# Kernel tuning notes

Measured on AMD Instinct MI355X. Metric: run time of the kernel, lower is better.

Reference implementation:

```python
import jax, jax.numpy as jnp
import numpy as np

N_HEAD = 16
N_EMBD = 1024
HEAD_DIM = N_EMBD // N_HEAD
ROPE_BASE = 10000.0


def _rms_norm(x):
    # F.rms_norm with eps=None uses dtype eps
    eps = jnp.finfo(x.dtype).eps
    ms = jnp.mean(jnp.square(x), axis=-1, keepdims=True)
    return x * jax.lax.rsqrt(ms + eps)


def _rope_tables(T, dtype):
    inv_freq = 1.0 / (ROPE_BASE ** (jnp.arange(0, HEAD_DIM, 2, dtype=jnp.float32) / HEAD_DIM))
    t = jnp.arange(T, dtype=jnp.float32)
    freqs = jnp.outer(t, inv_freq)  # [T, D/2]
    cos = jnp.cos(freqs).astype(dtype)[None, :, None, :]  # [1,T,1,D/2]
    sin = jnp.sin(freqs).astype(dtype)[None, :, None, :]
    return cos, sin


def _apply_rotary(x, cos, sin):
    d = x.shape[-1] // 2
    x1, x2 = x[..., :d], x[..., d:]
    y1 = x1 * cos + x2 * sin
    y2 = -x1 * sin + x2 * cos
    return jnp.concatenate([y1, y2], axis=-1).astype(x.dtype)


def setup_inputs() -> dict:
    key = jax.random.key(0)
    ks = jax.random.split(key, 7)
    B, T, C = 4, 2048, N_EMBD
    s = 0.02
    return {
        "x": jax.random.normal(ks[0], (B, T, C), dtype=jnp.float32),
        "v1": jax.random.normal(ks[1], (B, T, C), dtype=jnp.float32),
        "Wq": jax.random.normal(ks[2], (C, C), dtype=jnp.float32) * s,
        "Wk": jax.random.normal(ks[3], (C, C), dtype=jnp.float32) * s,
        "Wv": jax.random.normal(ks[4], (C, C), dtype=jnp.float32) * s,
        "Wproj": jax.random.normal(ks[5], (C, C), dtype=jnp.float32) * s,
        "lamb": jnp.float32(0.5),
    }


def reference(x, v1, Wq, Wk, Wv, Wproj, lamb):
    B, T, C = x.shape
    H, D = N_HEAD, HEAD_DIM
    q = (x @ Wq.T).reshape(B, T, H, D)
    k = (x @ Wk.T).reshape(B, T, H, D)
    v = (x @ Wv.T).reshape(B, T, H, D)
    # value-lambda residual mix
    v = (1.0 - lamb) * v + lamb * v1.reshape(B, T, H, D)
    # RMSNorm then RoPE on q, k
    cos, sin = _rope_tables(T, x.dtype)
    q = _apply_rotary(_rms_norm(q), cos, sin)
    k = _apply_rotary(_rms_norm(k), cos, sin)
    # causal SDPA
    scale = 1.0 / jnp.sqrt(jnp.float32(D)).astype(x.dtype)
    scores = jnp.einsum("bthd,bshd->bhts", q, k) * scale  # [B,H,T,T]
    causal = jnp.tril(jnp.ones((T, T), dtype=bool))
    scores = jnp.where(causal[None, None], scores, jnp.finfo(scores.dtype).min)
    attn = jax.nn.softmax(scores, axis=-1)
    y = jnp.einsum("bhts,bshd->bthd", attn, v).reshape(B, T, C)
    y = y @ Wproj.T
    return (y, v1)
```

## Files before the change

kernel.cpp:

```cpp
#include <hip/hip_runtime.h>
#include <hip/hip_bf16.h>

typedef __bf16 bf16x8 __attribute__((ext_vector_type(8)));
typedef __bf16 bf16x4 __attribute__((ext_vector_type(4)));
typedef float  f32x4  __attribute__((ext_vector_type(4)));
typedef unsigned u32x4 __attribute__((ext_vector_type(4)));

#define B_ 4
#define T_ 2048
#define H_ 16
#define D_ 64
#define C_ 1024
#define M_ 8192
#define NE_ ((size_t)M_ * C_)
#define KVSTR_ 2048

__global__ void probe_dtype(const unsigned short* __restrict__ x,
                            int* __restrict__ flag)
{
  __shared__ float red[256];
  float m = 0.0f;
  for (int i = threadIdx.x; i < 4096; i += 256) {
    unsigned int u = ((unsigned int)x[i]) << 16;
    float v = fabsf(__uint_as_float(u));
    if (!(v <= 1e30f)) v = 1e31f;
    m = fmaxf(m, v);
  }
  red[threadIdx.x] = m;
  __syncthreads();
  for (int s = 128; s > 0; s >>= 1) {
    if (threadIdx.x < s) red[threadIdx.x] = fmaxf(red[threadIdx.x], red[threadIdx.x + s]);
    __syncthreads();
  }
  if (threadIdx.x == 0) *flag = (red[0] > 100.0f) ? 1 : 0;
}

__device__ __forceinline__ float load1_adapt(const void* p, size_t idx, int f)
{
  if (f) return ((const float*)p)[idx];
  return __bfloat162float(((const __hip_bfloat16*)p)[idx]);
}

__global__ __launch_bounds__(256) void cvt_bf16(
    const int* __restrict__ flagp, const void* __restrict__ src,
    __bf16* __restrict__ dst, int n)
{
  const int f = *flagp;
  for (size_t i = ((size_t)blockIdx.x * 256 + threadIdx.x) * 8; i < (size_t)n;
       i += (size_t)gridDim.x * 2048) {
    bf16x8 r;
    if (f) {
      const float* pf = (const float*)src + i;
      float4 a = *(const float4*)pf;
      float4 b = *(const float4*)(pf + 4);
      r[0] = (__bf16)a.x; r[1] = (__bf16)a.y; r[2] = (__bf16)a.z; r[3] = (__bf16)a.w;
      r[4] = (__bf16)b.x; r[5] = (__bf16)b.y; r[6] = (__bf16)b.z; r[7] = (__bf16)b.w;
    } else {
      r = *(const bf16x8*)((const __bf16*)src + i);
    }
    *(bf16x8*)(dst + i) = r;
  }
}

__device__ __forceinline__ void g2lds16(const __bf16* g, __bf16* l)
{
  __builtin_amdgcn_global_load_lds(
      (const __attribute__((address_space(1))) void*)g,
      (__attribute__((address_space(3))) void*)l, 16, 0, 0);
}

__device__ __forceinline__ unsigned cvtpk_bf16(float lo, float hi)
{
  unsigned r;
  asm("v_cvt_pk_bf16_f32 %0, %1, %2" : "=v"(r) : "v"(lo), "v"(hi));
  return r;
}

__global__ __launch_bounds__(256) void gemm128(
    const __bf16* __restrict__ A, const __bf16* __restrict__ Bm,
    void* __restrict__ C, int M, int N, int K,
    const int* __restrict__ flagp, int adaptive)
{
  __shared__ __bf16 As[128][64];
  __shared__ __bf16 Bs[128][64];

  const int tid  = threadIdx.x;
  const int wv   = tid >> 6;
  const int lane = tid & 63;
  const int n16  = lane & 15;
  const int quad = lane >> 4;
  const int wm = (wv & 1) * 64, wn = (wv >> 1) * 64;

  const int nwgx = gridDim.x;
  const int id   = blockIdx.y * nwgx + blockIdx.x;
  const int cpx  = (nwgx * gridDim.y) >> 3;
  const int swz  = (id & 7) * cpx + (id >> 3);
  const int m0 = (swz % nwgx) * 128, n0 = (swz / nwgx) * 128;

  f32x4 acc[4][4];
#pragma unroll
  for (int i = 0; i < 4; i++)
#pragma unroll
    for (int j = 0; j < 4; j++) acc[i][j] = (f32x4){0.f, 0.f, 0.f, 0.f};

  const int trow = tid >> 3;
  const int tcol = (tid & 7) * 8;

  for (int k0 = 0; k0 < K; k0 += 64) {
#pragma unroll
    for (int p = 0; p < 4; p++) {
      g2lds16(A  + (size_t)(m0 + trow + p * 32) * K + k0 + tcol,
              &As[trow + p * 32][tcol]);
      g2lds16(Bm + (size_t)(n0 + trow + p * 32) * K + k0 + tcol,
              &Bs[trow + p * 32][tcol]);
    }
    __syncthreads();

#pragma unroll
    for (int kk = 0; kk < 2; kk++) {
      bf16x8 af[4], bf[4];
#pragma unroll
      for (int i = 0; i < 4; i++) {
        af[i] = *(const bf16x8*)&As[wm + i * 16 + n16][kk * 32 + quad * 8];
        bf[i] = *(const bf16x8*)&Bs[wn + i * 16 + n16][kk * 32 + quad * 8];
      }
#pragma unroll
      for (int i = 0; i < 4; i++)
#pragma unroll
        for (int j = 0; j < 4; j++)
          acc[i][j] = __builtin_amdgcn_mfma_f32_16x16x32_bf16(af[i], bf[j],
                                                              acc[i][j], 0, 0, 0);
    }
    __syncthreads();
  }

  const int f = adaptive ? *flagp : 0;
  const int rb = quad * 4;
#pragma unroll
  for (int i = 0; i < 4; i++)
#pragma unroll
    for (int j = 0; j < 4; j++)
#pragma unroll
      for (int r = 0; r < 4; r++) {
        const size_t idx = (size_t)(m0 + wm + i * 16 + rb + r) * N
                           + n0 + wn + j * 16 + n16;
        if (f) ((float*)C)[idx] = acc[i][j][r];
        else   ((__bf16*)C)[idx] = (__bf16)acc[i][j][r];
      }
}

__global__ __launch_bounds__(256) void fuse_rope_vmix(
    const int* __restrict__ flagp,
    __hip_bfloat16* __restrict__ q,
    __hip_bfloat16* __restrict__ kv,
    const void* __restrict__ v1,
    const void* __restrict__ lambp)
{
  const int f    = *flagp;
  const int task = blockIdx.x * 4 + (threadIdx.x >> 6);
  const int lane = threadIdx.x & 63;
  const int h  = task & 15;
  const int bt = task >> 4;
  const int t  = bt & (T_ - 1);
  const size_t baseq = (size_t)bt * C_ + h * D_ + lane;
  const size_t basek = (size_t)bt * KVSTR_ + h * D_ + lane;

  const int j = lane & 31;
  const float inv = expf(-(float)j * (9.2103403719761836f / 32.0f));
  const float ang = (float)t * inv;
  const float cs = cosf(ang), sn = sinf(ang);
  const float EPS = 0.0078125f;

  {
    float xv = __bfloat162float(q[baseq]);
    float ss = xv * xv;
#pragma unroll
    for (int off = 32; off >= 1; off >>= 1) ss += __shfl_xor(ss, off);
    float r  = rsqrtf(ss * (1.0f / 64.0f) + EPS);
    float xn = xv * r;
    float pr = __shfl_xor(xn, 32);
    float yv = (lane < 32) ? (xn * cs + pr * sn) : (pr * -sn + xn * cs);
    q[baseq] = __float2bfloat16(yv);
  }
  {
    float xv = __bfloat162float(kv[basek]);
    float ss = xv * xv;
#pragma unroll
    for (int off = 32; off >= 1; off >>= 1) ss += __shfl_xor(ss, off);
    float r  = rsqrtf(ss * (1.0f / 64.0f) + EPS);
    float xn = xv * r;
    float pr = __shfl_xor(xn, 32);
    float yv = (lane < 32) ? (xn * cs + pr * sn) : (pr * -sn + xn * cs);
    kv[basek] = __float2bfloat16(yv);
  }
  {
    float lam = load1_adapt(lambp, 0, f);
    float vv  = __bfloat162float(kv[basek + 1024]);
    float v1v = load1_adapt(v1, baseq, f);
    kv[basek + 1024] = __float2bfloat16((1.0f - lam) * vv + lam * v1v);
  }
}

__global__ __launch_bounds__(256) void transp_v(
    const __bf16* __restrict__ kv, __bf16* __restrict__ vt)
{
  __shared__ __bf16 Ts[64][72];
  const int bh = blockIdx.y;
  const int t0 = blockIdx.x * 64;
  const int b = bh >> 4, h = bh & 15;

  const int r = threadIdx.x >> 2;
  const int c = (threadIdx.x & 3) * 16;
  const __bf16* src = kv + (size_t)(b * T_ + t0 + r) * KVSTR_ + 1024 + h * D_ + c;
  *(bf16x8*)&Ts[r][c]     = *(const bf16x8*)src;
  *(bf16x8*)&Ts[r][c + 8] = *(const bf16x8*)(src + 8);
  __syncthreads();

  const int d  = threadIdx.x >> 2;
  const int tc = (threadIdx.x & 3) * 16;
  bf16x8 o0, o1;
#pragma unroll
  for (int jj = 0; jj < 8; jj++) { o0[jj] = Ts[tc + jj][d]; o1[jj] = Ts[tc + 8 + jj][d]; }
  __bf16* dst = vt + (size_t)(bh * D_ + d) * T_ + t0 + tc;
  *(bf16x8*)dst       = o0;
  *(bf16x8*)(dst + 8) = o1;
}

__device__ __forceinline__ void attn_tile(
    const bf16x8 (&KF)[4][2], const bf16x8 (&VF)[4][2],
    const bf16x8 (&aq)[2][2], f32x4 (&Ot)[2][4], float (&l_lane)[2],
    int s0, int rbase0, int n16, int quad, int srcA, int srcB, bool lowq)
{
#pragma unroll
  for (int rt = 0; rt < 2; rt++) {
    const int rbase = rbase0 + rt * 16;
    if (s0 <= rbase + 15) {
      f32x4 S[4];
      __builtin_amdgcn_s_setprio(1);
#pragma unroll
      for (int t = 0; t < 4; t++) {
        S[t] = (f32x4){0.f, 0.f, 0.f, 0.f};
        S[t] = __builtin_amdgcn_mfma_f32_16x16x32_bf16(KF[t][0], aq[rt][0], S[t], 0, 0, 0);
        S[t] = __builtin_amdgcn_mfma_f32_16x16x32_bf16(KF[t][1], aq[rt][1], S[t], 0, 0, 0);
      }
      __builtin_amdgcn_s_setprio(0);

      if (s0 + 63 > rbase) {
        const int tg = rbase + n16;
#pragma unroll
        for (int t = 0; t < 4; t++) {
#pragma unroll
          for (int r = 0; r < 4; r++) {
            const int sg = s0 + t * 16 + quad * 4 + r;
            if (sg > tg) S[t][r] = -1e30f;
          }
        }
      }

      float p[4][4];
#pragma unroll
      for (int t = 0; t < 4; t++)
#pragma unroll
        for (int r = 0; r < 4; r++)
          p[t][r] = __expf(S[t][r] - 8.0f);
      l_lane[rt] += ((p[0][0] + p[0][1]) + (p[0][2] + p[0][3]))
                  + ((p[1][0] + p[1][1]) + (p[1][2] + p[1][3]))
                  + ((p[2][0] + p[2][1]) + (p[2][2] + p[2][3]))
                  + ((p[3][0] + p[3][1]) + (p[3][2] + p[3][3]));

      unsigned pk0[4], pk1[4];
#pragma unroll
      for (int t = 0; t < 4; t++) {
        pk0[t] = cvtpk_bf16(p[t][0], p[t][1]);
        pk1[t] = cvtpk_bf16(p[t][2], p[t][3]);
      }

      bf16x8 pf[2];
#pragma unroll
      for (int c = 0; c < 2; c++) {
        const int tE = 2 * c, tO = 2 * c + 1;
        unsigned a0 = (unsigned)__shfl((int)pk0[tE], srcA);
        unsigned a1 = (unsigned)__shfl((int)pk0[tO], srcA);
        unsigned b0 = (unsigned)__shfl((int)pk1[tE], srcA);
        unsigned b1 = (unsigned)__shfl((int)pk1[tO], srcA);
        unsigned c0 = (unsigned)__shfl((int)pk0[tE], srcB);
        unsigned c1 = (unsigned)__shfl((int)pk0[tO], srcB);
        unsigned d0 = (unsigned)__shfl((int)pk1[tE], srcB);
        unsigned d1 = (unsigned)__shfl((int)pk1[tO], srcB);
        union { u32x4 u; bf16x8 bv; } uw;
        uw.u[0] = lowq ? a0 : a1;
        uw.u[1] = lowq ? b0 : b1;
        uw.u[2] = lowq ? c0 : c1;
        uw.u[3] = lowq ? d0 : d1;
        pf[c] = uw.bv;
      }

      __builtin_amdgcn_s_setprio(1);
#pragma unroll
      for (int t = 0; t < 4; t++) {
        Ot[rt][t] = __builtin_amdgcn_mfma_f32_16x16x32_bf16(VF[t][0], pf[0], Ot[rt][t], 0, 0, 0);
        Ot[rt][t] = __builtin_amdgcn_mfma_f32_16x16x32_bf16(VF[t][1], pf[1], Ot[rt][t], 0, 0, 0);
      }
      __builtin_amdgcn_s_setprio(0);
    }
  }
}

__global__ __launch_bounds__(256, 2) void attn_mfma(
    const __bf16* q,
    const __bf16* __restrict__ kv,
    const __bf16* __restrict__ vt,
    __bf16* y)
{
  const int tid  = threadIdx.x;
  const int wv   = tid >> 6;
  const int lane = tid & 63;
  const int n16  = lane & 15;
  const int quad = lane >> 4;

  const int id = blockIdx.y * gridDim.x + blockIdx.x;
  const int bh = (id & 7) + 8 * ((id >> 3) & 7);
  const int bx = id >> 6;
  const int b = bh >> 4, h = bh & 15;
  const int q0 = (gridDim.x - 1 - bx) * 128;
  const size_t hb  = (size_t)b * T_ * C_ + h * D_;
  const size_t hbk = (size_t)b * T_ * KVSTR_ + h * D_;
  const size_t vhb = (size_t)bh * D_ * T_;

  bf16x8 aq[2][2];
#pragma unroll
  for (int rt = 0; rt < 2; rt++) {
    const size_t qoff = hb + (size_t)(q0 + wv * 32 + rt * 16 + n16) * C_;
    aq[rt][0] = *(const bf16x8*)(q + qoff + quad * 8);
    aq[rt][1] = *(const bf16x8*)(q + qoff + 32 + quad * 8);
#pragma unroll
    for (int jj = 0; jj < 8; jj++) {
      aq[rt][0][jj] = (__bf16)((float)aq[rt][0][jj] * 0.125f);
      aq[rt][1][jj] = (__bf16)((float)aq[rt][1][jj] * 0.125f);
    }
  }

  f32x4 Ot[2][4];
  float l_lane[2];
#pragma unroll
  for (int rt = 0; rt < 2; rt++) {
    l_lane[rt] = 0.0f;
#pragma unroll
    for (int t = 0; t < 4; t++) Ot[rt][t] = (f32x4){0.f, 0.f, 0.f, 0.f};
  }

  const int srcA = n16 + 32 * (quad & 1);
  const int srcB = srcA + 16;
  const bool lowq = quad < 2;

  const int rbase0 = q0 + wv * 32;
  const int niter  = (rbase0 + 31) / 64 + 1;

#define LOADF(KF, VF, S0_)                                                   \
  do {                                                                       \
    _Pragma("unroll")                                                        \
    for (int t = 0; t < 4; t++) {                                            \
      const __bf16* kp = kv + hbk + (size_t)((S0_) + t * 16 + n16) * KVSTR_; \
      KF[t][0] = *(const bf16x8*)(kp + quad * 8);                            \
      KF[t][1] = *(const bf16x8*)(kp + 32 + quad * 8);                       \
      const __bf16* vp = vt + vhb + (size_t)(t * 16 + n16) * T_ + (S0_);     \
      VF[t][0] = *(const bf16x8*)(vp + quad * 8);                            \
      VF[t][1] = *(const bf16x8*)(vp + 32 + quad * 8);                       \
    }                                                                        \
  } while (0)

  bf16x8 kfA[4][2], vfA[4][2], kfB[4][2], vfB[4][2];
  LOADF(kfA, vfA, 0);

  int it = 0;
  for (;;) {
    int s0 = it * 64;
    bool hn = (it + 1 < niter);
    if (hn) LOADF(kfB, vfB, s0 + 64);
    attn_tile(kfA, vfA, aq, Ot, l_lane, s0, rbase0, n16, quad, srcA, srcB, lowq);
    if (!hn) break;
    ++it;
    s0 = it * 64;
    hn = (it + 1 < niter);
    if (hn) LOADF(kfA, vfA, s0 + 64);
    attn_tile(kfB, vfB, aq, Ot, l_lane, s0, rbase0, n16, quad, srcA, srcB, lowq);
    if (!hn) break;
    ++it;
  }
#undef LOADF

#pragma unroll
  for (int rt = 0; rt < 2; rt++) {
    float lt = l_lane[rt];
    lt += __shfl_xor(lt, 16);
    lt += __shfl_xor(lt, 32);
    const float linv = 1.0f / lt;
    const int qrow = q0 + wv * 32 + rt * 16 + n16;
#pragma unroll
    for (int t = 0; t < 4; t++) {
      bf16x4 o;
#pragma unroll
      for (int r = 0; r < 4; r++) o[r] = (__bf16)(Ot[rt][t][r] * linv);
      *(bf16x4*)(y + hb + (size_t)qrow * C_ + t * 16 + quad * 4) = o;
    }
  }
}

__global__ __launch_bounds__(256) void copy_v1(
    const int* __restrict__ flagp, const void* __restrict__ v1, void* __restrict__ out)
{
  const int f = *flagp;
  const size_t nbytes = NE_ * (f ? 4u : 2u);
  const uint4* s = (const uint4*)v1;
  uint4* d = (uint4*)((char*)out + nbytes);
  const size_t n16 = nbytes / 16;
  for (size_t i = (size_t)blockIdx.x * 256 + threadIdx.x; i < n16;
       i += (size_t)gridDim.x * 256)
    d[i] = s[i];
}

extern "C" void kernel_launch(void* const* d_in, const int* in_sizes, int n_in,
                              void* d_out, int out_size, void* d_ws, size_t ws_size,
                              hipStream_t stream)
{
  const void* x    = d_in[0];
  const void* v1   = d_in[1];
  const void* Wq   = d_in[2];
  const void* Wk   = d_in[3];
  const void* Wv   = d_in[4];
  const void* Wp   = d_in[5];
  const void* lamb = d_in[6];

  __bf16* xb  = (__bf16*)d_ws;
  __bf16* qw  = xb + NE_;
  __bf16* wqb = qw + NE_;
  __bf16* wkb = wqb + (size_t)C_ * C_;
  __bf16* wvb = wkb + (size_t)C_ * C_;
  __bf16* wpb = wvb + (size_t)C_ * C_;
  int* flagp  = (int*)(wpb + (size_t)C_ * C_);
  __bf16* vtb = xb;
  __bf16* kvw = (__bf16*)d_out;

  probe_dtype<<<1, 256, 0, stream>>>((const unsigned short*)x, flagp);

  cvt_bf16<<<4096, 256, 0, stream>>>(flagp, x,  xb,  (int)NE_);
  cvt_bf16<<<512,  256, 0, stream>>>(flagp, Wq, wqb, C_ * C_);
  cvt_bf16<<<512,  256, 0, stream>>>(flagp, Wk, wkb, C_ * C_);
  cvt_bf16<<<512,  256, 0, stream>>>(flagp, Wv, wvb, C_ * C_);
  cvt_bf16<<<512,  256, 0, stream>>>(flagp, Wp, wpb, C_ * C_);

  gemm128<<<dim3(M_ / 128, 8),  256, 0, stream>>>(xb, wqb, qw,  M_, 1024, C_, flagp, 0);
  gemm128<<<dim3(M_ / 128, 16), 256, 0, stream>>>(xb, wkb, kvw, M_, 2048, C_, flagp, 0);

  fuse_rope_vmix<<<(M_ * H_) / 4, 256, 0, stream>>>(
      flagp, (__hip_bfloat16*)qw, (__hip_bfloat16*)kvw, v1, lamb);

  transp_v<<<dim3(T_ / 64, B_ * H_), 256, 0, stream>>>(kvw, vtb);

  attn_mfma<<<dim3(T_ / 128, B_ * H_), 256, 0, stream>>>(qw, kvw, vtb, qw);

  gemm128<<<dim3(M_ / 128, 8), 256, 0, stream>>>(qw, wpb, d_out, M_, 1024, C_, flagp, 1);
  copy_v1<<<8192, 256, 0, stream>>>(flagp, v1, d_out);
}
```

Before: 452.3 us.

## Switch attention to 32x32x16 MFMA tiles with permlane32 swap for P

Rewrites the attention inner loop so each wave uses 32x32x16 bf16 MFMA instructions in place of 16x16x32, covering 32 query rows per wave with one accumulator pair. The P matrix is re-laid out for the PV product with v_permlane32_swap in place of eight cross-lane shuffles. Occupancy is raised to 3 blocks per SIMD via launch bounds. The explicit A/B register double-buffering of K/V loads is dropped in favour of a plain loop, which removes the software prefetch overlap and may expose load latency.

```diff
diff --git a/kernel.cpp b/kernel.cpp
--- a/kernel.cpp
+++ b/kernel.cpp
@@ -4,6 +4,7 @@
 typedef __bf16 bf16x8 __attribute__((ext_vector_type(8)));
 typedef __bf16 bf16x4 __attribute__((ext_vector_type(4)));
 typedef float  f32x4  __attribute__((ext_vector_type(4)));
+typedef float  f32x16 __attribute__((ext_vector_type(16)));
 typedef unsigned u32x4 __attribute__((ext_vector_type(4)));
 
 #define B_ 4
@@ -226,87 +227,7 @@
   *(bf16x8*)(dst + 8) = o1;
 }
 
-__device__ __forceinline__ void attn_tile(
-    const bf16x8 (&KF)[4][2], const bf16x8 (&VF)[4][2],
-    const bf16x8 (&aq)[2][2], f32x4 (&Ot)[2][4], float (&l_lane)[2],
-    int s0, int rbase0, int n16, int quad, int srcA, int srcB, bool lowq)
-{
-#pragma unroll
-  for (int rt = 0; rt < 2; rt++) {
-    const int rbase = rbase0 + rt * 16;
-    if (s0 <= rbase + 15) {
-      f32x4 S[4];
-      __builtin_amdgcn_s_setprio(1);
-#pragma unroll
-      for (int t = 0; t < 4; t++) {
-        S[t] = (f32x4){0.f, 0.f, 0.f, 0.f};
-        S[t] = __builtin_amdgcn_mfma_f32_16x16x32_bf16(KF[t][0], aq[rt][0], S[t], 0, 0, 0);
-        S[t] = __builtin_amdgcn_mfma_f32_16x16x32_bf16(KF[t][1], aq[rt][1], S[t], 0, 0, 0);
-      }
-      __builtin_amdgcn_s_setprio(0);
-
-      if (s0 + 63 > rbase) {
-        const int tg = rbase + n16;
-#pragma unroll
-        for (int t = 0; t < 4; t++) {
-#pragma unroll
-          for (int r = 0; r < 4; r++) {
-            const int sg = s0 + t * 16 + quad * 4 + r;
-            if (sg > tg) S[t][r] = -1e30f;
-          }
-        }
-      }
-
-      float p[4][4];
-#pragma unroll
-      for (int t = 0; t < 4; t++)
-#pragma unroll
-        for (int r = 0; r < 4; r++)
-          p[t][r] = __expf(S[t][r] - 8.0f);
-      l_lane[rt] += ((p[0][0] + p[0][1]) + (p[0][2] + p[0][3]))
-                  + ((p[1][0] + p[1][1]) + (p[1][2] + p[1][3]))
-                  + ((p[2][0] + p[2][1]) + (p[2][2] + p[2][3]))
-                  + ((p[3][0] + p[3][1]) + (p[3][2] + p[3][3]));
-
-      unsigned pk0[4], pk1[4];
-#pragma unroll
-      for (int t = 0; t < 4; t++) {
-        pk0[t] = cvtpk_bf16(p[t][0], p[t][1]);
-        pk1[t] = cvtpk_bf16(p[t][2], p[t][3]);
-      }
-
-      bf16x8 pf[2];
-#pragma unroll
-      for (int c = 0; c < 2; c++) {
-        const int tE = 2 * c, tO = 2 * c + 1;
-        unsigned a0 = (unsigned)__shfl((int)pk0[tE], srcA);
-        unsigned a1 = (unsigned)__shfl((int)pk0[tO], srcA);
-        unsigned b0 = (unsigned)__shfl((int)pk1[tE], srcA);
-        unsigned b1 = (unsigned)__shfl((int)pk1[tO], srcA);
-        unsigned c0 = (unsigned)__shfl((int)pk0[tE], srcB);
-        unsigned c1 = (unsigned)__shfl((int)pk0[tO], srcB);
-        unsigned d0 = (unsigned)__shfl((int)pk1[tE], srcB);
-        unsigned d1 = (unsigned)__shfl((int)pk1[tO], srcB);
-        union { u32x4 u; bf16x8 bv; } uw;
-        uw.u[0] = lowq ? a0 : a1;
-        uw.u[1] = lowq ? b0 : b1;
-        uw.u[2] = lowq ? c0 : c1;
-        uw.u[3] = lowq ? d0 : d1;
-        pf[c] = uw.bv;
-      }
-
-      __builtin_amdgcn_s_setprio(1);
-#pragma unroll
-      for (int t = 0; t < 4; t++) {
-        Ot[rt][t] = __builtin_amdgcn_mfma_f32_16x16x32_bf16(VF[t][0], pf[0], Ot[rt][t], 0, 0, 0);
-        Ot[rt][t] = __builtin_amdgcn_mfma_f32_16x16x32_bf16(VF[t][1], pf[1], Ot[rt][t], 0, 0, 0);
-      }
-      __builtin_amdgcn_s_setprio(0);
-    }
-  }
-}
-
-__global__ __launch_bounds__(256, 2) void attn_mfma(
+__global__ __launch_bounds__(256, 3) void attn_mfma(
     const __bf16* q,
     const __bf16* __restrict__ kv,
     const __bf16* __restrict__ vt,
@@ -315,8 +236,8 @@
   const int tid  = threadIdx.x;
   const int wv   = tid >> 6;
   const int lane = tid & 63;
-  const int n16  = lane & 15;
-  const int quad = lane >> 4;
+  const int l31  = lane & 31;
+  const int hi   = lane >> 5;
 
   const int id = blockIdx.y * gridDim.x + blockIdx.x;
   const int bh = (id & 7) + 8 * ((id >> 3) & 7);
@@ -327,82 +248,118 @@
   const size_t hbk = (size_t)b * T_ * KVSTR_ + h * D_;
   const size_t vhb = (size_t)bh * D_ * T_;
 
-  bf16x8 aq[2][2];
-#pragma unroll
-  for (int rt = 0; rt < 2; rt++) {
-    const size_t qoff = hb + (size_t)(q0 + wv * 32 + rt * 16 + n16) * C_;
-    aq[rt][0] = *(const bf16x8*)(q + qoff + quad * 8);
-    aq[rt][1] = *(const bf16x8*)(q + qoff + 32 + quad * 8);
-#pragma unroll
-    for (int jj = 0; jj < 8; jj++) {
-      aq[rt][0][jj] = (__bf16)((float)aq[rt][0][jj] * 0.125f);
-      aq[rt][1][jj] = (__bf16)((float)aq[rt][1][jj] * 0.125f);
-    }
-  }
-
-  f32x4 Ot[2][4];
-  float l_lane[2];
-#pragma unroll
-  for (int rt = 0; rt < 2; rt++) {
-    l_lane[rt] = 0.0f;
-#pragma unroll
-    for (int t = 0; t < 4; t++) Ot[rt][t] = (f32x4){0.f, 0.f, 0.f, 0.f};
-  }
-
-  const int srcA = n16 + 32 * (quad & 1);
-  const int srcB = srcA + 16;
-  const bool lowq = quad < 2;
-
-  const int rbase0 = q0 + wv * 32;
-  const int niter  = (rbase0 + 31) / 64 + 1;
-
-#define LOADF(KF, VF, S0_)                                                   \
-  do {                                                                       \
-    _Pragma("unroll")                                                        \
-    for (int t = 0; t < 4; t++) {                                            \
-      const __bf16* kp = kv + hbk + (size_t)((S0_) + t * 16 + n16) * KVSTR_; \
-      KF[t][0] = *(const bf16x8*)(kp + quad * 8);                            \
-      KF[t][1] = *(const bf16x8*)(kp + 32 + quad * 8);                       \
-      const __bf16* vp = vt + vhb + (size_t)(t * 16 + n16) * T_ + (S0_);     \
-      VF[t][0] = *(const bf16x8*)(vp + quad * 8);                            \
-      VF[t][1] = *(const bf16x8*)(vp + 32 + quad * 8);                       \
-    }                                                                        \
-  } while (0)
-
-  bf16x8 kfA[4][2], vfA[4][2], kfB[4][2], vfB[4][2];
-  LOADF(kfA, vfA, 0);
-
-  int it = 0;
-  for (;;) {
-    int s0 = it * 64;
-    bool hn = (it + 1 < niter);
-    if (hn) LOADF(kfB, vfB, s0 + 64);
-    attn_tile(kfA, vfA, aq, Ot, l_lane, s0, rbase0, n16, quad, srcA, srcB, lowq);
-    if (!hn) break;
-    ++it;
-    s0 = it * 64;
-    hn = (it + 1 < niter);
-    if (hn) LOADF(kfA, vfA, s0 + 64);
-    attn_tile(kfB, vfB, aq, Ot, l_lane, s0, rbase0, n16, quad, srcA, srcB, lowq);
-    if (!hn) break;
-    ++it;
-  }
-#undef LOADF
-
-#pragma unroll
-  for (int rt = 0; rt < 2; rt++) {
-    float lt = l_lane[rt];
-    lt += __shfl_xor(lt, 16);
-    lt += __shfl_xor(lt, 32);
-    const float linv = 1.0f / lt;
-    const int qrow = q0 + wv * 32 + rt * 16 + n16;
-#pragma unroll
-    for (int t = 0; t < 4; t++) {
-      bf16x4 o;
-#pragma unroll
-      for (int r = 0; r < 4; r++) o[r] = (__bf16)(Ot[rt][t][r] * linv);
-      *(bf16x4*)(y + hb + (size_t)qrow * C_ + t * 16 + quad * 4) = o;
-    }
+  const int qbase = q0 + wv * 32;
+
+  bf16x8 aq[4];
+  {
+    const __bf16* qp = q + hb + (size_t)(qbase + l31) * C_ + hi * 8;
+#pragma unroll
+    for (int i = 0; i < 4; i++) {
+      aq[i] = *(const bf16x8*)(qp + 16 * i);
+#pragma unroll
+      for (int jj = 0; jj < 8; jj++)
+        aq[i][jj] = (__bf16)((float)aq[i][jj] * 0.125f);
+    }
+  }
+
+  f32x16 Ot0, Ot1;
+#pragma unroll
+  for (int r = 0; r < 16; r++) { Ot0[r] = 0.f; Ot1[r] = 0.f; }
+  float l_lane = 0.f;
+
+  const int niter = (qbase + 31) / 64 + 1;
+  for (int it = 0; it < niter; it++) {
+    const int s0 = it * 64;
+    const int nst = (s0 + 32 <= qbase + 31) ? 2 : 1;
+
+    bf16x8 kf[2][4];
+#pragma unroll
+    for (int st = 0; st < 2; st++) {
+      const __bf16* kp = kv + hbk + (size_t)(s0 + 32 * st + l31) * KVSTR_ + hi * 8;
+#pragma unroll
+      for (int i = 0; i < 4; i++) kf[st][i] = *(const bf16x8*)(kp + 16 * i);
+    }
+    bf16x8 vf[2][4];
+#pragma unroll
+    for (int dh = 0; dh < 2; dh++) {
+      const __bf16* vp = vt + vhb + (size_t)(32 * dh + l31) * T_ + s0 + hi * 8;
+#pragma unroll
+      for (int sc = 0; sc < 4; sc++) vf[dh][sc] = *(const bf16x8*)(vp + 16 * sc);
+    }
+
+    bf16x8 pf[4];
+#pragma unroll
+    for (int st = 0; st < 2; st++) {
+      if (st < nst) {
+        f32x16 S;
+#pragma unroll
+        for (int r = 0; r < 16; r++) S[r] = 0.f;
+        __builtin_amdgcn_s_setprio(1);
+#pragma unroll
+        for (int i = 0; i < 4; i++)
+          S = __builtin_amdgcn_mfma_f32_32x32x16_bf16(kf[st][i], aq[i], S, 0, 0, 0);
+        __builtin_amdgcn_s_setprio(0);
+
+        if (s0 + 32 * st + 31 > qbase) {
+          const int tg = qbase + l31;
+#pragma unroll
+          for (int r = 0; r < 16; r++) {
+            const int sg = s0 + 32 * st + (r & 3) + 8 * (r >> 2) + 4 * hi;
+            if (sg > tg) S[r] = -1e30f;
+          }
+        }
+
+        float p[16];
+#pragma unroll
+        for (int r = 0; r < 16; r++) p[r] = __expf(S[r] - 8.0f);
+#pragma unroll
+        for (int r = 0; r < 16; r++) l_lane += p[r];
+
+        unsigned wg[4][2];
+#pragma unroll
+        for (int g = 0; g < 4; g++) {
+          wg[g][0] = cvtpk_bf16(p[4 * g + 0], p[4 * g + 1]);
+          wg[g][1] = cvtpk_bf16(p[4 * g + 2], p[4 * g + 3]);
+        }
+
+#pragma unroll
+        for (int scl = 0; scl < 2; scl++) {
+          unsigned x0 = wg[2 * scl][0], y0 = wg[2 * scl + 1][0];
+          unsigned x1 = wg[2 * scl][1], y1 = wg[2 * scl + 1][1];
+          asm volatile("v_permlane32_swap_b32 %0, %1" : "+v"(x0), "+v"(y0));
+          asm volatile("v_permlane32_swap_b32 %0, %1" : "+v"(x1), "+v"(y1));
+          union { u32x4 u; bf16x8 v8; } uw;
+          uw.u[0] = x0; uw.u[1] = x1; uw.u[2] = y0; uw.u[3] = y1;
+          pf[2 * st + scl] = uw.v8;
+        }
+      }
+    }
+
+    const int nsc = 2 * nst;
+    __builtin_amdgcn_s_setprio(1);
+#pragma unroll
+    for (int sc = 0; sc < 4; sc++)
+      if (sc < nsc) {
+        Ot0 = __builtin_amdgcn_mfma_f32_32x32x16_bf16(vf[0][sc], pf[sc], Ot0, 0, 0, 0);
+        Ot1 = __builtin_amdgcn_mfma_f32_32x32x16_bf16(vf[1][sc], pf[sc], Ot1, 0, 0, 0);
+      }
+    __builtin_amdgcn_s_setprio(0);
+  }
+
+  l_lane += __shfl_xor(l_lane, 32);
+  const float linv = 1.0f / l_lane;
+  const int qrow = qbase + l31;
+#pragma unroll
+  for (int g = 0; g < 4; g++) {
+    bf16x4 o0, o1;
+#pragma unroll
+    for (int m = 0; m < 4; m++) {
+      o0[m] = (__bf16)(Ot0[4 * g + m] * linv);
+      o1[m] = (__bf16)(Ot1[4 * g + m] * linv);
+    }
+    const int d0 = 8 * g + 4 * hi;
+    *(bf16x4*)(y + hb + (size_t)qrow * C_ + d0)      = o0;
+    *(bf16x4*)(y + hb + (size_t)qrow * C_ + 32 + d0) = o1;
   }
 }
 
```

Measured after the change: 444.0 us. No clear change (-1.8%).
